# Optimization experiments

Hardware: AMD Instinct MI355X
Metric: run time of the kernel (lower is better)

## Reference

```python
import jax, jax.numpy as jnp
import numpy as np

B, T, D = 4, 4096, 2048
K = 1024
H, KVH, HD = 16, 4, 128
FF = 8192
EPS = 1e-6


def _rmsnorm(x, w):
    v = jnp.mean(x * x, axis=-1, keepdims=True)
    return x * jax.lax.rsqrt(v + EPS) * w


def _rotate_half(x):
    x1, x2 = jnp.split(x, 2, axis=-1)
    return jnp.concatenate([-x2, x1], axis=-1)


def setup_inputs() -> dict:
    key = jax.random.key(0)
    ks = jax.random.split(key, 16)
    hidden_states = jax.random.normal(ks[0], (B, T, D), dtype=jnp.float32)
    # unique sorted indices per sequence (top-k selection without duplicates)
    scores = jax.random.uniform(ks[1], (B, T))
    topk_indices = jnp.sort(jax.lax.top_k(scores, K)[1], axis=-1).astype(jnp.int64)
    gating_scores = jax.random.uniform(ks[2], (B, K), dtype=jnp.float32)
    # rotary embeddings over the full sequence [B, T, HD]
    inv = 1.0 / (10000.0 ** (jnp.arange(0, HD, 2, dtype=jnp.float32) / HD))
    ang = jnp.arange(T, dtype=jnp.float32)[:, None] * inv[None, :]  # [T, HD/2]
    emb = jnp.concatenate([ang, ang], axis=-1)
    cos = jnp.broadcast_to(jnp.cos(emb)[None], (B, T, HD)).astype(jnp.float32)
    sin = jnp.broadcast_to(jnp.sin(emb)[None], (B, T, HD)).astype(jnp.float32)
    s = 0.02
    params = dict(
        Wq=jax.random.normal(ks[3], (D, H * HD)) * s,
        bq=jnp.zeros((H * HD,)),
        Wk=jax.random.normal(ks[4], (D, KVH * HD)) * s,
        bk=jnp.zeros((KVH * HD,)),
        Wv=jax.random.normal(ks[5], (D, KVH * HD)) * s,
        bv=jnp.zeros((KVH * HD,)),
        Wo=jax.random.normal(ks[6], (H * HD, D)) * s,
        w_gate=jax.random.normal(ks[7], (D, FF)) * s,
        w_up=jax.random.normal(ks[8], (D, FF)) * s,
        w_down=jax.random.normal(ks[9], (FF, D)) * s,
        ln1_w=jnp.ones((D,)),
        ln2_w=jnp.ones((D,)),
    )
    return dict(hidden_states=hidden_states, topk_indices=topk_indices,
                gating_scores=gating_scores, cos=cos, sin=sin, **params)


def _decoder_layer(x, cos_s, sin_s, Wq, bq, Wk, bk, Wv, bv, Wo,
                   w_gate, w_up, w_down, ln1_w, ln2_w):
    # x: [B, K, D]; cos_s/sin_s: [B, K, HD]
    res = x
    h = _rmsnorm(x, ln1_w)
    q = (h @ Wq + bq).reshape(B, K, H, HD)
    k = (h @ Wk + bk).reshape(B, K, KVH, HD)
    v = (h @ Wv + bv).reshape(B, K, KVH, HD)
    c = cos_s[:, :, None, :]
    s = sin_s[:, :, None, :]
    q = q * c + _rotate_half(q) * s
    k = k * c + _rotate_half(k) * s
    # GQA: repeat kv heads
    k = jnp.repeat(k, H // KVH, axis=2)
    v = jnp.repeat(v, H // KVH, axis=2)
    scores = jnp.einsum('bqhd,bkhd->bhqk', q, k) / np.sqrt(HD)
    causal = jnp.tril(jnp.ones((K, K), dtype=bool))
    scores = jnp.where(causal[None, None], scores, jnp.finfo(scores.dtype).min)
    attn = jax.nn.softmax(scores, axis=-1)
    out = jnp.einsum('bhqk,bkhd->bqhd', attn, v).reshape(B, K, H * HD)
    x = res + out @ Wo
    # MLP (SwiGLU)
    res = x
    h = _rmsnorm(x, ln2_w)
    x = res + (jax.nn.silu(h @ w_gate) * (h @ w_up)) @ w_down
    return x


def reference(hidden_states, topk_indices, gating_scores, cos, sin,
              Wq, bq, Wk, bk, Wv, bv, Wo, w_gate, w_up, w_down, ln1_w, ln2_w):
    idx = topk_indices[:, :, None]  # [B, K, 1]
    selected = jnp.take_along_axis(hidden_states, idx, axis=1)  # [B, K, D]
    cos_s = jnp.take_along_axis(cos, idx, axis=1)
    sin_s = jnp.take_along_axis(sin, idx, axis=1)
    processed = _decoder_layer(selected, cos_s, sin_s, Wq, bq, Wk, bk, Wv, bv,
                               Wo, w_gate, w_up, w_down, ln1_w, ln2_w)
    # soft gating: selected + gate * (processed - selected)
    updated = selected + (processed - selected) * gating_scores[:, :, None]
    b_idx = jnp.arange(B)[:, None]
    final = hidden_states.at[b_idx, topk_indices].set(updated)
    return final
```

## Files before the change

kernel.cpp:

```cpp
#include <hip/hip_runtime.h>
#include <stdint.h>

typedef __bf16 bf16;
typedef __attribute__((ext_vector_type(8))) __bf16 bf16x8;
typedef __attribute__((ext_vector_type(4))) float f32x4;

namespace {

constexpr int cB = 4, cT = 4096, cD = 2048, cK = 1024, cH = 16, cKVH = 4, cHD = 128, cFF = 8192;
constexpr int cM = cB * cK;
constexpr int QKVW = cH * cHD + 2 * cKVH * cHD;

__device__ __forceinline__ void load_lds16(const void* g, void* l) {
  __builtin_amdgcn_global_load_lds((const __attribute__((address_space(1))) void*)g,
                                   (__attribute__((address_space(3))) void*)l, 16, 0, 0);
}

template <int N>
__device__ __forceinline__ void waitcnt_vm() {
  if constexpr (N == 0) asm volatile("s_waitcnt vmcnt(0)" ::: "memory");
  else if constexpr (N == 3) asm volatile("s_waitcnt vmcnt(3)" ::: "memory");
  else if constexpr (N == 4) asm volatile("s_waitcnt vmcnt(4)" ::: "memory");
  else if constexpr (N == 6) asm volatile("s_waitcnt vmcnt(6)" ::: "memory");
  else if constexpr (N == 8) asm volatile("s_waitcnt vmcnt(8)" ::: "memory");
  else if constexpr (N == 9) asm volatile("s_waitcnt vmcnt(9)" ::: "memory");
  else if constexpr (N == 12) asm volatile("s_waitcnt vmcnt(12)" ::: "memory");
  else static_assert(N == 0, "unsupported vmcnt literal");
}

template <int OP>
__device__ __forceinline__ float blk_reduce(float v) {
  __shared__ float sm[5];
  const int tid = threadIdx.x, lane = tid & 63, wid = tid >> 6;
#pragma unroll
  for (int o = 32; o; o >>= 1) {
    float o2 = __shfl_down(v, o, 64);
    v = OP ? fmaxf(v, o2) : v + o2;
  }
  if (lane == 0) sm[wid] = v;
  __syncthreads();
  if (tid == 0) {
    float r = sm[0];
#pragma unroll
    for (int i = 1; i < 4; ++i) r = OP ? fmaxf(r, sm[i]) : r + sm[i];
    sm[4] = r;
  }
  __syncthreads();
  float r = sm[4];
  __syncthreads();
  return r;
}

template <int BN, int WM, int WN, int RING, int UNROLL, class Epi>
__global__ __launch_bounds__(512, 2)
void gemm256(const bf16* __restrict__ A, int lda,
             const bf16* __restrict__ Bm, int ldb,
             int Kd, int GM, Epi epi) {
  constexpr int BM = 256;
  constexpr int FM = BM / WM / 16;
  constexpr int FN = BN / WN / 16;
  constexpr int ACALLS = 2;
  constexpr int BCALLS = BN / 128;
  constexpr int L = ACALLS + BCALLS;
  constexpr int D = RING - 1;
  constexpr int SLOTA = BM * 64;
  constexpr int SLOTB = BN * 64;
  constexpr int SLOT = SLOTA + SLOTB;
  __shared__ __align__(16) char lds[RING * SLOT];

  const int tid = threadIdx.x;
  const int lane = tid & 63;
  const int wid = tid >> 6;
  const int l15 = lane & 15, lq = lane >> 4;
  const int wr = wid / WN, wc = wid % WN;

  const int nwg = gridDim.x;
  const int xcd = blockIdx.x & 7, loc = blockIdx.x >> 3;
  const int wg = xcd * (nwg >> 3) + loc;
  const int GN = nwg / GM;
  const int per = 8 * GN;
  const int g = wg / per, r = wg % per;
  const int bm = g * 8 + (r & 7);
  const int bn = r >> 3;

  const bf16* Abase = A + (int64_t)bm * BM * lda;
  const bf16* Bbase = Bm + (int64_t)bn * BN * ldb;

  const bf16* srcA[ACALLS];
  int dstA[ACALLS];
#pragma unroll
  for (int c2 = 0; c2 < ACALLS; ++c2) {
    const int chunk = c2 * 512 + tid;
    const int row = chunk >> 2, pc = chunk & 3;
    const int lc = pc ^ ((row >> 1) & 3);
    srcA[c2] = Abase + (int64_t)row * lda + lc * 8;
    dstA[c2] = chunk * 16;
  }
  const bf16* srcB[BCALLS];
  int dstB[BCALLS];
#pragma unroll
  for (int c2 = 0; c2 < BCALLS; ++c2) {
    const int chunk = c2 * 512 + tid;
    const int row = chunk >> 2, pc = chunk & 3;
    const int lc = pc ^ ((row >> 1) & 3);
    srcB[c2] = Bbase + (int64_t)row * ldb + lc * 8;
    dstB[c2] = chunk * 16;
  }

  int offA[FM], offB[FN];
#pragma unroll
  for (int m = 0; m < FM; ++m) {
    const int row = wr * (BM / WM) + m * 16 + l15;
    offA[m] = row * 64 + (lq ^ ((row >> 1) & 3)) * 16;
  }
#pragma unroll
  for (int n = 0; n < FN; ++n) {
    const int row = wc * (BN / WN) + n * 16 + l15;
    offB[n] = SLOTA + row * 64 + (lq ^ ((row >> 1) & 3)) * 16;
  }

  const int KT = Kd >> 5;
  auto stage = [&](int t) {
    char* sb = lds + (size_t)(t % RING) * SLOT;
#pragma unroll
    for (int c2 = 0; c2 < ACALLS; ++c2)
      load_lds16(srcA[c2] + t * 32, sb + dstA[c2]);
#pragma unroll
    for (int c2 = 0; c2 < BCALLS; ++c2)
      load_lds16(srcB[c2] + t * 32, sb + SLOTA + dstB[c2]);
  };
  auto compute = [&](int t, f32x4 (&acc)[FM][FN]) {
    const char* sb = lds + (size_t)(t % RING) * SLOT;
    bf16x8 av[FM], bv[FN];
#pragma unroll
    for (int m = 0; m < FM; ++m) av[m] = *(const bf16x8*)(sb + offA[m]);
#pragma unroll
    for (int n = 0; n < FN; ++n) bv[n] = *(const bf16x8*)(sb + offB[n]);
    __builtin_amdgcn_s_setprio(1);
#pragma unroll
    for (int m = 0; m < FM; ++m)
#pragma unroll
      for (int n = 0; n < FN; ++n)
        acc[m][n] = __builtin_amdgcn_mfma_f32_16x16x32_bf16(av[m], bv[n], acc[m][n], 0, 0, 0);
    __builtin_amdgcn_s_setprio(0);
  };

  f32x4 acc[FM][FN] = {};

  if constexpr (UNROLL == 1) {
#pragma unroll
    for (int i = 0; i < D; ++i) stage(i);
    waitcnt_vm<(D - 1) * L>();
    __builtin_amdgcn_s_barrier();
    __builtin_amdgcn_sched_barrier(0);
    for (int t = 0; t < KT - D; ++t) {
      stage(t + D);
      compute(t, acc);
      waitcnt_vm<(D - 1) * L>();
      __builtin_amdgcn_s_barrier();
      __builtin_amdgcn_sched_barrier(0);
    }
    waitcnt_vm<0>();
    __builtin_amdgcn_s_barrier();
    for (int t = KT - D; t < KT; ++t) compute(t, acc);
  } else {
    static_assert(RING == 5 && UNROLL == 2, "pair mode is RING=5");
#pragma unroll
    for (int i = 0; i < 3; ++i) stage(i);
    waitcnt_vm<L>();
    __builtin_amdgcn_s_barrier();
    __builtin_amdgcn_sched_barrier(0);
    int t = 0;
    for (; t <= KT - 6; t += 2) {
      stage(t + 3);
      stage(t + 4);
      compute(t, acc);
      compute(t + 1, acc);
      waitcnt_vm<L>();
      __builtin_amdgcn_s_barrier();
      __builtin_amdgcn_sched_barrier(0);
    }
    stage(KT - 1);
    waitcnt_vm<0>();
    __builtin_amdgcn_s_barrier();
    compute(KT - 4, acc);
    compute(KT - 3, acc);
    compute(KT - 2, acc);
    compute(KT - 1, acc);
  }

#pragma unroll
  for (int m = 0; m < FM; ++m) {
    const int r0 = bm * BM + wr * (BM / WM) + m * 16 + lq * 4;
#pragma unroll
    for (int n = 0; n < FN; ++n) {
      const int c1 = bn * BN + wc * (BN / WN) + n * 16 + l15;
#pragma unroll
      for (int j = 0; j < 4; ++j) epi(r0 + j, c1, acc[m][n][j]);
    }
  }
}

__global__ __launch_bounds__(512, 2)
void gemm_gateup(const bf16* __restrict__ A, const bf16* __restrict__ Bg,
                 const bf16* __restrict__ Bu, bf16* __restrict__ act) {
  constexpr int BM = 256;
  constexpr int SLOTA = BM * 64;
  __shared__ __align__(16) char lds[4 * SLOTA];

  const int tid = threadIdx.x;
  const int lane = tid & 63;
  const int wid = tid >> 6;
  const int l15 = lane & 15, lq = lane >> 4;
  const int wr = wid >> 2, wc = wid & 3;

  const int nwg = gridDim.x;
  const int xcd = blockIdx.x & 7, loc = blockIdx.x >> 3;
  const int wg = xcd * (nwg >> 3) + loc;
  const int GM = 16, GN = nwg / GM;
  const int per = 8 * GN;
  const int gg = wg / per, r = wg % per;
  const int bm = gg * 8 + (r & 7);
  const int bn = r >> 3;

  const bf16* Abase = A + (int64_t)bm * BM * cD;

  const bf16* srcA[2];
  int dstA[2];
#pragma unroll
  for (int c2 = 0; c2 < 2; ++c2) {
    const int chunk = c2 * 512 + tid;
    const int row = chunk >> 2, pc = chunk & 3;
    const int lc = pc ^ ((row >> 1) & 3);
    srcA[c2] = Abase + (int64_t)row * cD + lc * 8;
    dstA[c2] = chunk * 16;
  }

  const int rk0 = bn * 128 + wc * 32 + l15;
  const bf16* pG = Bg + (int64_t)rk0 * cD + lq * 8;
  const bf16* pU = Bu + (int64_t)rk0 * cD + lq * 8;

  int offA[8];
#pragma unroll
  for (int m = 0; m < 8; ++m) {
    const int row = wr * 128 + m * 16 + l15;
    offA[m] = row * 64 + (lq ^ ((row >> 1) & 3)) * 16;
  }

  const int KT = cD >> 5;
  auto stageA = [&](int t) {
    char* sb = lds + (size_t)(t & 3) * SLOTA;
    load_lds16(srcA[0] + t * 32, sb + dstA[0]);
    load_lds16(srcA[1] + t * 32, sb + dstA[1]);
  };

  f32x4 accg[8][2] = {}, accu[8][2] = {};

  stageA(0);
  stageA(1);
  for (int t = 0; t < KT; ++t) {
    bf16x8 gfr0 = *(const bf16x8*)(pG + t * 32);
    bf16x8 gfr1 = *(const bf16x8*)(pG + t * 32 + 16 * cD);
    bf16x8 ufr0 = *(const bf16x8*)(pU + t * 32);
    bf16x8 ufr1 = *(const bf16x8*)(pU + t * 32 + 16 * cD);
    asm volatile("" ::: "memory");
    if (t + 2 < KT) stageA(t + 2);
    asm volatile("" ::: "memory");
    waitcnt_vm<8>();
    __builtin_amdgcn_s_barrier();
    asm volatile("" ::: "memory");
    const char* sb = lds + (size_t)(t & 3) * SLOTA;
    bf16x8 av[8];
#pragma unroll
    for (int m = 0; m < 8; ++m) av[m] = *(const bf16x8*)(sb + offA[m]);
    __builtin_amdgcn_s_setprio(1);
#pragma unroll
    for (int m = 0; m < 8; ++m) {
      accg[m][0] = __builtin_amdgcn_mfma_f32_16x16x32_bf16(av[m], gfr0, accg[m][0], 0, 0, 0);
      accg[m][1] = __builtin_amdgcn_mfma_f32_16x16x32_bf16(av[m], gfr1, accg[m][1], 0, 0, 0);
      accu[m][0] = __builtin_amdgcn_mfma_f32_16x16x32_bf16(av[m], ufr0, accu[m][0], 0, 0, 0);
      accu[m][1] = __builtin_amdgcn_mfma_f32_16x16x32_bf16(av[m], ufr1, accu[m][1], 0, 0, 0);
    }
    __builtin_amdgcn_s_setprio(0);
  }

#pragma unroll
  for (int m = 0; m < 8; ++m) {
    const int r0 = bm * BM + wr * 128 + m * 16 + lq * 4;
#pragma unroll
    for (int n = 0; n < 2; ++n) {
      const int c1 = bn * 128 + wc * 32 + n * 16 + l15;
#pragma unroll
      for (int j = 0; j < 4; ++j) {
        float gv = accg[m][n][j];
        float s = gv / (1.f + __expf(-gv));
        act[(int64_t)(r0 + j) * cFF + c1] = (bf16)(s * accu[m][n][j]);
      }
    }
  }
}

struct EpiQKV {
  bf16* out; const float* bias;
  __device__ void operator()(int r, int c, float v) const {
    out[(int64_t)r * QKVW + c] = (bf16)(v + bias[c]);
  }
};
struct EpiOProj {
  float* x; const float* hidden; const int* topk;
  __device__ void operator()(int r, int c, float v) const {
    int b = r >> 10;
    int t = topk[r];
    x[(int64_t)r * cD + c] = v + hidden[((int64_t)b * cT + t) * cD + c];
  }
};
struct EpiDown {
  float* out; const float* x; const float* hidden; const int* topk; const float* gating;
  __device__ void operator()(int r, int c, float v) const {
    int b = r >> 10;
    int t = topk[r];
    float x2 = v + x[(int64_t)r * cD + c];
    int64_t ho = ((int64_t)b * cT + t) * cD + c;
    float sel = hidden[ho];
    out[ho] = sel + (x2 - sel) * gating[r];
  }
};

__global__ __launch_bounds__(256, 2) void flash_attn(const bf16* __restrict__ qkv,
                                                     const bf16* __restrict__ vt,
                                                     bf16* __restrict__ outb) {
  constexpr int QB = 64, KVB = 128;
  __shared__ __align__(16) char lds[81920];
  char* sK = lds;
  char* sP = lds + 32768;
  char* sV = lds + 49152;

  const int qt = blockIdx.x, h = blockIdx.y, b = blockIdx.z;
  const int kvh = h >> 2;
  const int qlo = qt * QB;
  const int tid = threadIdx.x, lane = tid & 63, wid = tid >> 6;
  const int l15 = lane & 15, lq = lane >> 4;
  const int wid16 = wid * 16;

  const bf16* qbase = qkv + (int64_t)(b * cK + qlo) * QKVW + h * cHD;
  const bf16* kbase = qkv + (int64_t)(b * cK) * QKVW + cH * cHD + kvh * cHD;
  const bf16* vtbase = vt + (int64_t)(b * cKVH + kvh) * cHD * cK;

#pragma unroll
  for (int c2 = 0; c2 < 4; ++c2) {
    int chunk = c2 * 256 + tid;
    int row = chunk >> 4, c16 = chunk & 15;
    load_lds16(qbase + (int64_t)row * QKVW + (c16 ^ (row & 15)) * 8, sK + chunk * 16);
  }
  __syncthreads();
  bf16x8 qf[4];
  {
    const int row = wid16 + l15;
#pragma unroll
    for (int kt = 0; kt < 4; ++kt)
      qf[kt] = *(const bf16x8*)(sK + row * 256 + (((kt * 4 + lq) ^ (row & 15)) * 16));
  }
  __syncthreads();

  f32x4 oacc[8] = {};
  float m_run[4], l_run[4];
#pragma unroll
  for (int j = 0; j < 4; ++j) { m_run[j] = -3.0e38f; l_run[j] = 0.f; }

  const int jmax = (qlo + QB - 1) >> 7;
  const float sl2e = 0.08838834764831845f * 1.44269504088896f;

  for (int jj = 0; jj <= jmax; ++jj) {
#pragma unroll
    for (int c2 = 0; c2 < 8; ++c2) {
      int chunk = c2 * 256 + tid;
      int row = chunk >> 4, c16 = chunk & 15;
      int cs = (c16 ^ (row & 15)) * 8;
      load_lds16(kbase + (int64_t)(jj * KVB + row) * QKVW + cs, sK + chunk * 16);
      load_lds16(vtbase + (int64_t)row * cK + jj * KVB + cs, sV + chunk * 16);
    }
    __syncthreads();

    f32x4 sacc[8] = {};
#pragma unroll
    for (int kt = 0; kt < 4; ++kt) {
      bf16x8 bv[8];
#pragma unroll
      for (int n = 0; n < 8; ++n) {
        int rk = n * 16 + l15;
        bv[n] = *(const bf16x8*)(sK + rk * 256 + (((kt * 4 + lq) ^ (rk & 15)) * 16));
      }
#pragma unroll
      for (int n = 0; n < 8; ++n)
        sacc[n] = __builtin_amdgcn_mfma_f32_16x16x32_bf16(qf[kt], bv[n], sacc[n], 0, 0, 0);
    }

    if (jj == jmax) {
#pragma unroll
      for (int n = 0; n < 8; ++n)
#pragma unroll
        for (int j = 0; j < 4; ++j) {
          int qrow = qlo + wid16 + lq * 4 + j;
          int kcol = jj * KVB + n * 16 + l15;
          if (kcol > qrow) sacc[n][j] = -3.0e38f;
        }
    }

#pragma unroll
    for (int j = 0; j < 4; ++j) {
      float mx = sacc[0][j];
#pragma unroll
      for (int n = 1; n < 8; ++n) mx = fmaxf(mx, sacc[n][j]);
#pragma unroll
      for (int off = 1; off < 16; off <<= 1) mx = fmaxf(mx, __shfl_xor(mx, off, 64));
      float mnew = fmaxf(m_run[j], mx);
      float corr = exp2f((m_run[j] - mnew) * sl2e);
      m_run[j] = mnew;
      float ps = 0.f;
#pragma unroll
      for (int n = 0; n < 8; ++n) {
        float p = exp2f((sacc[n][j] - mnew) * sl2e);
        sacc[n][j] = p;
        ps += p;
      }
#pragma unroll
      for (int off = 1; off < 16; off <<= 1) ps += __shfl_xor(ps, off, 64);
      l_run[j] = l_run[j] * corr + ps;
#pragma unroll
      for (int n = 0; n < 8; ++n) oacc[n][j] *= corr;
    }

#pragma unroll
    for (int n = 0; n < 8; ++n)
#pragma unroll
      for (int j = 0; j < 4; ++j) {
        int row = wid16 + lq * 4 + j;
        int col = n * 16 + l15;
        int c16 = (col >> 3) ^ (row & 15);
        *(bf16*)(sP + row * 256 + c16 * 16 + (col & 7) * 2) = (bf16)sacc[n][j];
      }
    __syncthreads();

#pragma unroll
    for (int kt = 0; kt < 4; ++kt) {
      const int prow = wid16 + l15;
      bf16x8 av = *(const bf16x8*)(sP + prow * 256 + (((kt * 4 + lq) ^ (prow & 15)) * 16));
      bf16x8 bv[8];
#pragma unroll
      for (int n = 0; n < 8; ++n) {
        int rd = n * 16 + l15;
        bv[n] = *(const bf16x8*)(sV + rd * 256 + (((kt * 4 + lq) ^ (rd & 15)) * 16));
      }
#pragma unroll
      for (int n = 0; n < 8; ++n)
        oacc[n] = __builtin_amdgcn_mfma_f32_16x16x32_bf16(av, bv[n], oacc[n], 0, 0, 0);
    }
    __syncthreads();
  }

#pragma unroll
  for (int j = 0; j < 4; ++j) {
    int row = qlo + wid16 + lq * 4 + j;
    float inv = 1.f / l_run[j];
#pragma unroll
    for (int n = 0; n < 8; ++n) {
      int col = h * cHD + n * 16 + l15;
      outb[((int64_t)b * cK + row) * cD + col] = (bf16)(oacc[n][j] * inv);
    }
  }
}

__global__ void copy_skip(const float4* __restrict__ s, float4* __restrict__ d,
                          const unsigned char* __restrict__ flags, int64_t n) {
  int64_t i = (int64_t)blockIdx.x * blockDim.x + threadIdx.x;
  const int64_t st = (int64_t)gridDim.x * blockDim.x;
  for (; i < n; i += st) {
    int row = (int)(i >> 9);
    if (!flags[row]) d[i] = s[i];
  }
}

__global__ void build_flags(const int* __restrict__ topk, unsigned char* __restrict__ flags) {
  int r = blockIdx.x * 256 + threadIdx.x;
  if (r < cM) flags[(r >> 10) * cT + topk[r]] = 1;
}

__global__ void wconv(const float* __restrict__ src, bf16* __restrict__ dst,
                      int R, int C, int coff, int ldd) {
  __shared__ float t[32][33];
  const int c0 = blockIdx.x * 32, r0 = blockIdx.y * 32;
  for (int rr = threadIdx.y; rr < 32; rr += 8)
    t[rr][threadIdx.x] = src[(int64_t)(r0 + rr) * C + c0 + threadIdx.x];
  __syncthreads();
  for (int rr = threadIdx.y; rr < 32; rr += 8)
    dst[(int64_t)(c0 + rr + coff) * ldd + r0 + threadIdx.x] = (bf16)t[threadIdx.x][rr];
}

__global__ void biascat(const float* __restrict__ bq, const float* __restrict__ bk,
                        const float* __restrict__ bv, float* __restrict__ o) {
  int i = blockIdx.x * 256 + threadIdx.x;
  if (i < QKVW) o[i] = (i < 2048) ? bq[i] : (i < 2560 ? bk[i - 2048] : bv[i - 2560]);
}

__global__ void rmsnorm_rows(const float* __restrict__ base, const int* __restrict__ topk,
                             const float* __restrict__ w, bf16* __restrict__ out) {
  const int r = blockIdx.x;
  const float* src;
  if (topk) {
    int t = topk[r];
    src = base + ((int64_t)(r >> 10) * cT + t) * cD;
  } else {
    src = base + (int64_t)r * cD;
  }
  const int tid = threadIdx.x;
  const float4* s4 = (const float4*)src;
  float4 a = s4[tid * 2], b = s4[tid * 2 + 1];
  float ss = a.x * a.x + a.y * a.y + a.z * a.z + a.w * a.w +
             b.x * b.x + b.y * b.y + b.z * b.z + b.w * b.w;
  float tot = blk_reduce<0>(ss);
  float sc = rsqrtf(tot * (1.f / cD) + 1e-6f);
  bf16* o = out + (int64_t)r * cD;
  const int d0 = tid * 8;
  o[d0 + 0] = (bf16)(a.x * sc * w[d0 + 0]);
  o[d0 + 1] = (bf16)(a.y * sc * w[d0 + 1]);
  o[d0 + 2] = (bf16)(a.z * sc * w[d0 + 2]);
  o[d0 + 3] = (bf16)(a.w * sc * w[d0 + 3]);
  o[d0 + 4] = (bf16)(b.x * sc * w[d0 + 4]);
  o[d0 + 5] = (bf16)(b.y * sc * w[d0 + 5]);
  o[d0 + 6] = (bf16)(b.z * sc * w[d0 + 6]);
  o[d0 + 7] = (bf16)(b.w * sc * w[d0 + 7]);
}

__global__ void rope_kernel(bf16* __restrict__ qkv, const float* __restrict__ cosb,
                            const float* __restrict__ sinb, const int* __restrict__ topk) {
  const int r = blockIdx.x;
  const int b = r >> 10;
  const int t = topk[r];
  const float* cr = cosb + ((int64_t)b * cT + t) * cHD;
  const float* sr = sinb + ((int64_t)b * cT + t) * cHD;
  bf16* rowq = qkv + (int64_t)r * QKVW;
  for (int p = threadIdx.x; p < (cH + cKVH) * 64; p += 256) {
    int hh = p >> 6, d = p & 63;
    bf16* base = (hh < cH) ? (rowq + hh * cHD) : (rowq + cH * cHD + (hh - cH) * cHD);
    float x1 = (float)base[d], x2 = (float)base[d + 64];
    float c1 = cr[d], s1 = sr[d], c2 = cr[d + 64], s2 = sr[d + 64];
    base[d] = (bf16)(x1 * c1 - x2 * s1);
    base[d + 64] = (bf16)(x2 * c2 + x1 * s2);
  }
}

__global__ void vtrans(const bf16* __restrict__ qkv, bf16* __restrict__ Vt) {
  __shared__ bf16 t[32][33];
  const int bz = blockIdx.z, b = bz >> 2, kv = bz & 3;
  const int k0 = blockIdx.x * 32, d0 = blockIdx.y * 32;
  for (int rr = threadIdx.y; rr < 32; rr += 8)
    t[rr][threadIdx.x] =
        qkv[(int64_t)(b * cK + k0 + rr) * QKVW + cH * cHD + cKVH * cHD + kv * cHD + d0 + threadIdx.x];
  __syncthreads();
  for (int rr = threadIdx.y; rr < 32; rr += 8)
    Vt[((int64_t)(b * cKVH + kv) * cHD + d0 + rr) * cK + k0 + threadIdx.x] = t[threadIdx.x][rr];
}

}

extern "C" void kernel_launch(void* const* d_in, const int* in_sizes, int n_in,
                              void* d_out, int out_size, void* d_ws, size_t ws_size,
                              hipStream_t stream) {
  const float* hidden = (const float*)d_in[0];
  const int* topk = (const int*)d_in[1];
  const float* gating = (const float*)d_in[2];
  const float* cosb = (const float*)d_in[3];
  const float* sinb = (const float*)d_in[4];
  const float* Wq = (const float*)d_in[5];
  const float* bq = (const float*)d_in[6];
  const float* Wk = (const float*)d_in[7];
  const float* bk = (const float*)d_in[8];
  const float* Wv = (const float*)d_in[9];
  const float* bv = (const float*)d_in[10];
  const float* Wo = (const float*)d_in[11];
  const float* wg = (const float*)d_in[12];
  const float* wu = (const float*)d_in[13];
  const float* wd = (const float*)d_in[14];
  const float* ln1 = (const float*)d_in[15];
  const float* ln2 = (const float*)d_in[16];
  float* out = (float*)d_out;
  (void)in_sizes; (void)n_in; (void)out_size; (void)ws_size;

  char* ws = (char*)d_ws;
  size_t off = 0;
  auto alloc = [&](size_t bytes) {
    char* p = ws + off;
    off += (bytes + 255) & ~(size_t)255;
    return p;
  };
  bf16* wt_qkv = (bf16*)alloc((size_t)QKVW * cD * 2);
  bf16* wt_o = (bf16*)alloc((size_t)cD * cD * 2);
  bf16* wt_g = (bf16*)alloc((size_t)cFF * cD * 2);
  bf16* wt_u = (bf16*)alloc((size_t)cFF * cD * 2);
  bf16* wt_d = (bf16*)alloc((size_t)cD * cFF * 2);
  float* bias_cat = (float*)alloc((size_t)QKVW * 4);
  bf16* hbuf = (bf16*)alloc((size_t)cM * cD * 2);
  bf16* qkv = (bf16*)alloc((size_t)cM * QKVW * 2);
  bf16* vt = (bf16*)alloc((size_t)cB * cKVH * cHD * cK * 2);
  bf16* attnout = (bf16*)alloc((size_t)cM * cD * 2);
  float* xbuf = (float*)alloc((size_t)cM * cD * 4);
  bf16* actbuf = (bf16*)alloc((size_t)cM * cFF * 2);
  unsigned char* flags = (unsigned char*)alloc((size_t)cB * cT);

  hipMemsetAsync(flags, 0, (size_t)cB * cT, stream);
  build_flags<<<cM / 256, 256, 0, stream>>>(topk, flags);
  copy_skip<<<2048, 256, 0, stream>>>((const float4*)hidden, (float4*)out, flags,
                                      (int64_t)cB * cT * cD / 4);

  const dim3 tb(32, 8);
  wconv<<<dim3(cD / 32, cD / 32), tb, 0, stream>>>(Wq, wt_qkv, cD, cD, 0, cD);
  wconv<<<dim3(512 / 32, cD / 32), tb, 0, stream>>>(Wk, wt_qkv, cD, 512, 2048, cD);
  wconv<<<dim3(512 / 32, cD / 32), tb, 0, stream>>>(Wv, wt_qkv, cD, 512, 2560, cD);
  wconv<<<dim3(cD / 32, cD / 32), tb, 0, stream>>>(Wo, wt_o, cD, cD, 0, cD);
  wconv<<<dim3(cFF / 32, cD / 32), tb, 0, stream>>>(wg, wt_g, cD, cFF, 0, cD);
  wconv<<<dim3(cFF / 32, cD / 32), tb, 0, stream>>>(wu, wt_u, cD, cFF, 0, cD);
  wconv<<<dim3(cD / 32, cFF / 32), tb, 0, stream>>>(wd, wt_d, cFF, cD, 0, cFF);
  biascat<<<(QKVW + 255) / 256, 256, 0, stream>>>(bq, bk, bv, bias_cat);

  rmsnorm_rows<<<cM, 256, 0, stream>>>(hidden, topk, ln1, hbuf);
  gemm256<256, 2, 4, 5, 2, EpiQKV><<<16 * (QKVW / 256), 512, 0, stream>>>(
      hbuf, cD, wt_qkv, cD, cD, 16, EpiQKV{qkv, bias_cat});
  rope_kernel<<<cM, 256, 0, stream>>>(qkv, cosb, sinb, topk);
  vtrans<<<dim3(cK / 32, cHD / 32, cB * cKVH), tb, 0, stream>>>(qkv, vt);

  flash_attn<<<dim3(cK / 64, cH, cB), 256, 0, stream>>>(qkv, vt, attnout);

  gemm256<128, 4, 2, 5, 2, EpiOProj><<<16 * (cD / 128), 512, 0, stream>>>(
      attnout, cD, wt_o, cD, cD, 16, EpiOProj{xbuf, hidden, topk});
  rmsnorm_rows<<<cM, 256, 0, stream>>>(xbuf, nullptr, ln2, hbuf);
  gemm_gateup<<<16 * (cFF / 128), 512, 0, stream>>>(hbuf, wt_g, wt_u, actbuf);
  gemm256<128, 4, 2, 5, 2, EpiDown><<<16 * (cD / 128), 512, 0, stream>>>(
      actbuf, cFF, wt_d, cFF, cFF, 16, EpiDown{out, xbuf, hidden, topk, gating});
}
```

Measured before the change: 922.8 us.

## Pre-swizzle gate/up weights into MFMA fragment layout and double-buffer B loads

The gate/up weights are now converted into a fragment-contiguous bf16 layout, so each lane's 16-byte B fragment for a k-step sits next to its neighbours' and a wavefront reads fully coalesced 1KB blocks. The gate/up GEMM main loop is unrolled by two and uses ping-pong registers, issuing the next k-step's B loads before the current MFMAs run. The aim is to hide global-load latency and cut uncoalesced strided reads. The cost is a new conversion kernel with strided fp32 reads and more vector registers, and the waitcnt bookkeeping has to stay matched to the load counts.

```diff
diff --git a/kernel.cpp b/kernel.cpp
--- a/kernel.cpp
+++ b/kernel.cpp
@@ -236,9 +236,12 @@
     dstA[c2] = chunk * 16;
   }
 
-  const int rk0 = bn * 128 + wc * 32 + l15;
-  const bf16* pG = Bg + (int64_t)rk0 * cD + lq * 8;
-  const bf16* pU = Bu + (int64_t)rk0 * cD + lq * 8;
+  const int KT = cD >> 5;
+  const int nb0 = bn * 8 + wc * 2;
+  const bf16* pG0 = Bg + ((int64_t)nb0 * KT * 64 + lane) * 8;
+  const bf16* pG1 = Bg + ((int64_t)(nb0 + 1) * KT * 64 + lane) * 8;
+  const bf16* pU0 = Bu + ((int64_t)nb0 * KT * 64 + lane) * 8;
+  const bf16* pU1 = Bu + ((int64_t)(nb0 + 1) * KT * 64 + lane) * 8;
 
   int offA[8];
 #pragma unroll
@@ -247,7 +250,6 @@
     offA[m] = row * 64 + (lq ^ ((row >> 1) & 3)) * 16;
   }
 
-  const int KT = cD >> 5;
   auto stageA = [&](int t) {
     char* sb = lds + (size_t)(t & 3) * SLOTA;
     load_lds16(srcA[0] + t * 32, sb + dstA[0]);
@@ -255,33 +257,45 @@
   };
 
   f32x4 accg[8][2] = {}, accu[8][2] = {};
-
+  bf16x8 gA0, gA1, uA0, uA1, gB0, gB1, uB0, uB1;
+
+  auto loadB = [&](int t, bf16x8& g0, bf16x8& g1, bf16x8& u0, bf16x8& u1) {
+    g0 = *(const bf16x8*)(pG0 + (int64_t)t * 512);
+    g1 = *(const bf16x8*)(pG1 + (int64_t)t * 512);
+    u0 = *(const bf16x8*)(pU0 + (int64_t)t * 512);
+    u1 = *(const bf16x8*)(pU1 + (int64_t)t * 512);
+  };
+  auto mfma_step = [&](const char* sb, const bf16x8& g0, const bf16x8& g1,
+                       const bf16x8& u0, const bf16x8& u1) {
+    bf16x8 av[8];
+#pragma unroll
+    for (int m = 0; m < 8; ++m) av[m] = *(const bf16x8*)(sb + offA[m]);
+    __builtin_amdgcn_s_setprio(1);
+#pragma unroll
+    for (int m = 0; m < 8; ++m) {
+      accg[m][0] = __builtin_amdgcn_mfma_f32_16x16x32_bf16(av[m], g0, accg[m][0], 0, 0, 0);
+      accg[m][1] = __builtin_amdgcn_mfma_f32_16x16x32_bf16(av[m], g1, accg[m][1], 0, 0, 0);
+      accu[m][0] = __builtin_amdgcn_mfma_f32_16x16x32_bf16(av[m], u0, accu[m][0], 0, 0, 0);
+      accu[m][1] = __builtin_amdgcn_mfma_f32_16x16x32_bf16(av[m], u1, accu[m][1], 0, 0, 0);
+    }
+    __builtin_amdgcn_s_setprio(0);
+  };
+
+  loadB(0, gA0, gA1, uA0, uA1);
   stageA(0);
   stageA(1);
-  for (int t = 0; t < KT; ++t) {
-    bf16x8 gfr0 = *(const bf16x8*)(pG + t * 32);
-    bf16x8 gfr1 = *(const bf16x8*)(pG + t * 32 + 16 * cD);
-    bf16x8 ufr0 = *(const bf16x8*)(pU + t * 32);
-    bf16x8 ufr1 = *(const bf16x8*)(pU + t * 32 + 16 * cD);
-    asm volatile("" ::: "memory");
+  for (int t = 0; t < KT; t += 2) {
+    loadB(t + 1, gB0, gB1, uB0, uB1);
     if (t + 2 < KT) stageA(t + 2);
-    asm volatile("" ::: "memory");
     waitcnt_vm<8>();
     __builtin_amdgcn_s_barrier();
-    asm volatile("" ::: "memory");
-    const char* sb = lds + (size_t)(t & 3) * SLOTA;
-    bf16x8 av[8];
-#pragma unroll
-    for (int m = 0; m < 8; ++m) av[m] = *(const bf16x8*)(sb + offA[m]);
-    __builtin_amdgcn_s_setprio(1);
-#pragma unroll
-    for (int m = 0; m < 8; ++m) {
-      accg[m][0] = __builtin_amdgcn_mfma_f32_16x16x32_bf16(av[m], gfr0, accg[m][0], 0, 0, 0);
-      accg[m][1] = __builtin_amdgcn_mfma_f32_16x16x32_bf16(av[m], gfr1, accg[m][1], 0, 0, 0);
-      accu[m][0] = __builtin_amdgcn_mfma_f32_16x16x32_bf16(av[m], ufr0, accu[m][0], 0, 0, 0);
-      accu[m][1] = __builtin_amdgcn_mfma_f32_16x16x32_bf16(av[m], ufr1, accu[m][1], 0, 0, 0);
-    }
-    __builtin_amdgcn_s_setprio(0);
+    mfma_step(lds + (size_t)(t & 3) * SLOTA, gA0, gA1, uA0, uA1);
+    if (t + 2 < KT) loadB(t + 2, gA0, gA1, uA0, uA1);
+    if (t + 3 < KT) stageA(t + 3);
+    if (t + 3 < KT) waitcnt_vm<6>();
+    else            waitcnt_vm<4>();
+    __builtin_amdgcn_s_barrier();
+    mfma_step(lds + (size_t)((t + 1) & 3) * SLOTA, gB0, gB1, uB0, uB1);
   }
 
 #pragma unroll
@@ -494,6 +508,20 @@
   __syncthreads();
   for (int rr = threadIdx.y; rr < 32; rr += 8)
     dst[(int64_t)(c0 + rr + coff) * ldd + r0 + threadIdx.x] = (bf16)t[threadIdx.x][rr];
+}
+
+__global__ void wconv_frag(const float* __restrict__ src, bf16* __restrict__ dst,
+                           int N, int KT) {
+  const int id = blockIdx.x * 256 + threadIdx.x;
+  const int lane = id & 63;
+  const int frag = id >> 6;
+  const int kc = frag % KT;
+  const int nb = frag / KT;
+  const int l15 = lane & 15, lq = lane >> 4;
+  const float* s = src + (int64_t)(kc * 32 + lq * 8) * N + nb * 16 + l15;
+  bf16* o = dst + (int64_t)id * 8;
+#pragma unroll
+  for (int j = 0; j < 8; ++j) o[j] = (bf16)s[(int64_t)j * N];
 }
 
 __global__ void biascat(const float* __restrict__ bq, const float* __restrict__ bk,
@@ -617,8 +645,8 @@
   wconv<<<dim3(512 / 32, cD / 32), tb, 0, stream>>>(Wk, wt_qkv, cD, 512, 2048, cD);
   wconv<<<dim3(512 / 32, cD / 32), tb, 0, stream>>>(Wv, wt_qkv, cD, 512, 2560, cD);
   wconv<<<dim3(cD / 32, cD / 32), tb, 0, stream>>>(Wo, wt_o, cD, cD, 0, cD);
-  wconv<<<dim3(cFF / 32, cD / 32), tb, 0, stream>>>(wg, wt_g, cD, cFF, 0, cD);
-  wconv<<<dim3(cFF / 32, cD / 32), tb, 0, stream>>>(wu, wt_u, cD, cFF, 0, cD);
+  wconv_frag<<<(cFF / 16) * (cD / 32) * 64 / 256, 256, 0, stream>>>(wg, wt_g, cFF, cD / 32);
+  wconv_frag<<<(cFF / 16) * (cD / 32) * 64 / 256, 256, 0, stream>>>(wu, wt_u, cFF, cD / 32);
   wconv<<<dim3(cD / 32, cFF / 32), tb, 0, stream>>>(wd, wt_d, cFF, cD, 0, cFF);
   biascat<<<(QKVW + 255) / 256, 256, 0, stream>>>(bq, bk, bv, bias_cat);
 
```

New measurement: 855.9 us. -7.2%, faster.

## Rewrite gate/up GEMM with interleaved weights and LDS-staged 256x256 tiles

Applied to the files above, without the earlier changes.

The gate and up weights are converted into one interleaved bf16 matrix, with 16-row blocks of gate and up alternating. The gate/up GEMM is rewritten to stage both A and B tiles (256x256, K-step 64) into double-buffered swizzled LDS. Loads for the next step are interleaved with four MFMA quadrant phases separated by barriers. This replaces direct global B-fragment loads, improving B reuse across waves and hiding load latency, at the cost of more barriers and LDS use. The flash attention grid is also remapped so that blocks sharing a KV head are grouped per XCD for L2 locality.

```diff
diff --git a/kernel.cpp b/kernel.cpp
--- a/kernel.cpp
+++ b/kernel.cpp
@@ -19,12 +19,11 @@
 template <int N>
 __device__ __forceinline__ void waitcnt_vm() {
   if constexpr (N == 0) asm volatile("s_waitcnt vmcnt(0)" ::: "memory");
+  else if constexpr (N == 2) asm volatile("s_waitcnt vmcnt(2)" ::: "memory");
   else if constexpr (N == 3) asm volatile("s_waitcnt vmcnt(3)" ::: "memory");
   else if constexpr (N == 4) asm volatile("s_waitcnt vmcnt(4)" ::: "memory");
   else if constexpr (N == 6) asm volatile("s_waitcnt vmcnt(6)" ::: "memory");
   else if constexpr (N == 8) asm volatile("s_waitcnt vmcnt(8)" ::: "memory");
-  else if constexpr (N == 9) asm volatile("s_waitcnt vmcnt(9)" ::: "memory");
-  else if constexpr (N == 12) asm volatile("s_waitcnt vmcnt(12)" ::: "memory");
   else static_assert(N == 0, "unsupported vmcnt literal");
 }
 
@@ -202,14 +201,12 @@
 }
 
 __global__ __launch_bounds__(512, 2)
-void gemm_gateup(const bf16* __restrict__ A, const bf16* __restrict__ Bg,
-                 const bf16* __restrict__ Bu, bf16* __restrict__ act) {
-  constexpr int BM = 256;
-  constexpr int SLOTA = BM * 64;
-  __shared__ __align__(16) char lds[4 * SLOTA];
-
-  const int tid = threadIdx.x;
-  const int lane = tid & 63;
+void gemm_gateup8(const bf16* __restrict__ A, const bf16* __restrict__ Bgu,
+                  bf16* __restrict__ act) {
+  constexpr int QSZ = 64 * 128;
+  __shared__ __align__(16) char lds[2 * 8 * QSZ];
+
+  const int tid = threadIdx.x, lane = tid & 63;
   const int wid = tid >> 6;
   const int l15 = lane & 15, lq = lane >> 4;
   const int wr = wid >> 2, wc = wid & 3;
@@ -219,82 +216,111 @@
   const int wg = xcd * (nwg >> 3) + loc;
   const int GM = 16, GN = nwg / GM;
   const int per = 8 * GN;
-  const int gg = wg / per, r = wg % per;
-  const int bm = gg * 8 + (r & 7);
+  const int g = wg / per, r = wg % per;
+  const int bm = g * 8 + (r & 7);
   const int bn = r >> 3;
 
-  const bf16* Abase = A + (int64_t)bm * BM * cD;
-
-  const bf16* srcA[2];
-  int dstA[2];
-#pragma unroll
-  for (int c2 = 0; c2 < 2; ++c2) {
-    const int chunk = c2 * 512 + tid;
-    const int row = chunk >> 2, pc = chunk & 3;
-    const int lc = pc ^ ((row >> 1) & 3);
-    srcA[c2] = Abase + (int64_t)row * cD + lc * 8;
-    dstA[c2] = chunk * 16;
-  }
-
-  const int rk0 = bn * 128 + wc * 32 + l15;
-  const bf16* pG = Bg + (int64_t)rk0 * cD + lq * 8;
-  const bf16* pU = Bu + (int64_t)rk0 * cD + lq * 8;
-
-  int offA[8];
+  const bf16* Abase = A + (int64_t)bm * 256 * cD;
+  const bf16* Bbase = Bgu + (int64_t)bn * 256 * cD;
+
+  const int srow = tid >> 3, spc = tid & 7;
+  const int slc = spc ^ (srow & 7);
+  const int sdst = tid * 16;
+  const bf16* qsrc[8];
+#pragma unroll
+  for (int q = 0; q < 4; ++q) qsrc[q] = Abase + (int64_t)(q * 64 + srow) * cD + slc * 8;
+#pragma unroll
+  for (int q = 0; q < 4; ++q) qsrc[4 + q] = Bbase + (int64_t)(q * 64 + srow) * cD + slc * 8;
+
+  auto stageQ = [&](int buf, int q, int kt) {
+    load_lds16(qsrc[q] + kt * 64, lds + (size_t)(buf * 8 + q) * QSZ + sdst);
+  };
+
+  f32x4 acc[8][4] = {};
+  bf16x8 af[4][2], bfr[2][2];
+
+  auto ldA = [&](int buf, int qr) {
+    const char* qb = lds + (size_t)(buf * 8 + wr * 2 + qr) * QSZ;
+#pragma unroll
+    for (int mq = 0; mq < 4; ++mq) {
+      const int rr = mq * 16 + l15;
+#pragma unroll
+      for (int ks = 0; ks < 2; ++ks)
+        af[mq][ks] = *(const bf16x8*)(qb + rr * 128 + (((ks * 4 + lq) ^ (rr & 7)) * 16));
+    }
+  };
+  auto ldB = [&](int buf, int qc) {
+    const char* qb = lds + (size_t)(buf * 8 + 4 + wc) * QSZ;
+#pragma unroll
+    for (int nq = 0; nq < 2; ++nq) {
+      const int rr = qc * 32 + nq * 16 + l15;
+#pragma unroll
+      for (int ks = 0; ks < 2; ++ks)
+        bfr[nq][ks] = *(const bf16x8*)(qb + rr * 128 + (((ks * 4 + lq) ^ (rr & 7)) * 16));
+    }
+  };
+  auto mfma16 = [&](int qr, int qc) {
+    __builtin_amdgcn_s_setprio(1);
+#pragma unroll
+    for (int ks = 0; ks < 2; ++ks)
+#pragma unroll
+      for (int mq = 0; mq < 4; ++mq)
+#pragma unroll
+        for (int nq = 0; nq < 2; ++nq)
+          acc[qr * 4 + mq][qc * 2 + nq] = __builtin_amdgcn_mfma_f32_16x16x32_bf16(
+              af[mq][ks], bfr[nq][ks], acc[qr * 4 + mq][qc * 2 + nq], 0, 0, 0);
+    __builtin_amdgcn_s_setprio(0);
+  };
+
+  const int KT = cD >> 6;
+
+  stageQ(0, 4, 0); stageQ(0, 5, 0);
+  stageQ(0, 6, 0); stageQ(0, 7, 0);
+  stageQ(0, 0, 0); stageQ(0, 2, 0);
+  stageQ(0, 1, 0); stageQ(0, 3, 0);
+  waitcnt_vm<2>();
+  __builtin_amdgcn_s_barrier();
+
+  for (int t = 0; t < KT; ++t) {
+    const int buf = t & 1, nb = buf ^ 1;
+    const bool more = (t + 1 < KT);
+    ldA(buf, 0);
+    ldB(buf, 0);
+    if (more) { stageQ(nb, 4, t + 1); stageQ(nb, 5, t + 1); }
+    __builtin_amdgcn_s_barrier();
+    mfma16(0, 0);
+    __builtin_amdgcn_s_barrier();
+    ldB(buf, 1);
+    if (more) { stageQ(nb, 6, t + 1); stageQ(nb, 7, t + 1); }
+    __builtin_amdgcn_s_barrier();
+    mfma16(0, 1);
+    if (more) waitcnt_vm<4>();
+    else      waitcnt_vm<0>();
+    __builtin_amdgcn_s_barrier();
+    ldA(buf, 1);
+    if (more) { stageQ(nb, 0, t + 1); stageQ(nb, 2, t + 1); }
+    __builtin_amdgcn_s_barrier();
+    mfma16(1, 1);
+    __builtin_amdgcn_s_barrier();
+    ldB(buf, 0);
+    if (more) { stageQ(nb, 1, t + 1); stageQ(nb, 3, t + 1); }
+    __builtin_amdgcn_s_barrier();
+    mfma16(1, 0);
+    if (more) waitcnt_vm<2>();
+    __builtin_amdgcn_s_barrier();
+  }
+
 #pragma unroll
   for (int m = 0; m < 8; ++m) {
-    const int row = wr * 128 + m * 16 + l15;
-    offA[m] = row * 64 + (lq ^ ((row >> 1) & 3)) * 16;
-  }
-
-  const int KT = cD >> 5;
-  auto stageA = [&](int t) {
-    char* sb = lds + (size_t)(t & 3) * SLOTA;
-    load_lds16(srcA[0] + t * 32, sb + dstA[0]);
-    load_lds16(srcA[1] + t * 32, sb + dstA[1]);
-  };
-
-  f32x4 accg[8][2] = {}, accu[8][2] = {};
-
-  stageA(0);
-  stageA(1);
-  for (int t = 0; t < KT; ++t) {
-    bf16x8 gfr0 = *(const bf16x8*)(pG + t * 32);
-    bf16x8 gfr1 = *(const bf16x8*)(pG + t * 32 + 16 * cD);
-    bf16x8 ufr0 = *(const bf16x8*)(pU + t * 32);
-    bf16x8 ufr1 = *(const bf16x8*)(pU + t * 32 + 16 * cD);
-    asm volatile("" ::: "memory");
-    if (t + 2 < KT) stageA(t + 2);
-    asm volatile("" ::: "memory");
-    waitcnt_vm<8>();
-    __builtin_amdgcn_s_barrier();
-    asm volatile("" ::: "memory");
-    const char* sb = lds + (size_t)(t & 3) * SLOTA;
-    bf16x8 av[8];
-#pragma unroll
-    for (int m = 0; m < 8; ++m) av[m] = *(const bf16x8*)(sb + offA[m]);
-    __builtin_amdgcn_s_setprio(1);
-#pragma unroll
-    for (int m = 0; m < 8; ++m) {
-      accg[m][0] = __builtin_amdgcn_mfma_f32_16x16x32_bf16(av[m], gfr0, accg[m][0], 0, 0, 0);
-      accg[m][1] = __builtin_amdgcn_mfma_f32_16x16x32_bf16(av[m], gfr1, accg[m][1], 0, 0, 0);
-      accu[m][0] = __builtin_amdgcn_mfma_f32_16x16x32_bf16(av[m], ufr0, accu[m][0], 0, 0, 0);
-      accu[m][1] = __builtin_amdgcn_mfma_f32_16x16x32_bf16(av[m], ufr1, accu[m][1], 0, 0, 0);
-    }
-    __builtin_amdgcn_s_setprio(0);
-  }
-
-#pragma unroll
-  for (int m = 0; m < 8; ++m) {
-    const int r0 = bm * BM + wr * 128 + m * 16 + lq * 4;
-#pragma unroll
-    for (int n = 0; n < 2; ++n) {
-      const int c1 = bn * 128 + wc * 32 + n * 16 + l15;
+    const int row = bm * 256 + wr * 128 + (m >> 2) * 64 + (m & 3) * 16 + lq * 4;
+#pragma unroll
+    for (int p = 0; p < 2; ++p) {
+      const int col = bn * 128 + wc * 32 + p * 16 + l15;
 #pragma unroll
       for (int j = 0; j < 4; ++j) {
-        float gv = accg[m][n][j];
+        float gv = acc[m][2 * p][j];
         float s = gv / (1.f + __expf(-gv));
-        act[(int64_t)(r0 + j) * cFF + c1] = (bf16)(s * accu[m][n][j]);
+        act[(int64_t)(row + j) * cFF + col] = (bf16)(s * acc[m][2 * p + 1][j]);
       }
     }
   }
@@ -335,7 +361,9 @@
   char* sP = lds + 32768;
   char* sV = lds + 49152;
 
-  const int qt = blockIdx.x, h = blockIdx.y, b = blockIdx.z;
+  const int xcdid = blockIdx.x & 7, locid = blockIdx.x >> 3;
+  const int wg = xcdid * 128 + locid;
+  const int qt = wg & 15, h = (wg >> 4) & 15, b = wg >> 8;
   const int kvh = h >> 2;
   const int qlo = qt * QB;
   const int tid = threadIdx.x, lane = tid & 63, wid = tid >> 6;
@@ -494,6 +522,21 @@
   __syncthreads();
   for (int rr = threadIdx.y; rr < 32; rr += 8)
     dst[(int64_t)(c0 + rr + coff) * ldd + r0 + threadIdx.x] = (bf16)t[threadIdx.x][rr];
+}
+
+__global__ void wconv_gu(const float* __restrict__ srcG, const float* __restrict__ srcU,
+                         bf16* __restrict__ dst) {
+  __shared__ float t[32][33];
+  const float* src = blockIdx.z ? srcU : srcG;
+  const int c0 = blockIdx.x * 32, r0 = blockIdx.y * 32;
+  for (int rr = threadIdx.y; rr < 32; rr += 8)
+    t[rr][threadIdx.x] = src[(int64_t)(r0 + rr) * cFF + c0 + threadIdx.x];
+  __syncthreads();
+  for (int rr = threadIdx.y; rr < 32; rr += 8) {
+    int c = c0 + rr;
+    int dr = ((c & ~15) << 1) | (blockIdx.z ? 16 : 0) | (c & 15);
+    dst[(int64_t)dr * cD + r0 + threadIdx.x] = (bf16)t[threadIdx.x][rr];
+  }
 }
 
 __global__ void biascat(const float* __restrict__ bq, const float* __restrict__ bk,
@@ -595,8 +638,7 @@
   };
   bf16* wt_qkv = (bf16*)alloc((size_t)QKVW * cD * 2);
   bf16* wt_o = (bf16*)alloc((size_t)cD * cD * 2);
-  bf16* wt_g = (bf16*)alloc((size_t)cFF * cD * 2);
-  bf16* wt_u = (bf16*)alloc((size_t)cFF * cD * 2);
+  bf16* wt_gu = (bf16*)alloc((size_t)2 * cFF * cD * 2);
   bf16* wt_d = (bf16*)alloc((size_t)cD * cFF * 2);
   float* bias_cat = (float*)alloc((size_t)QKVW * 4);
   bf16* hbuf = (bf16*)alloc((size_t)cM * cD * 2);
@@ -607,7 +649,7 @@
   bf16* actbuf = (bf16*)alloc((size_t)cM * cFF * 2);
   unsigned char* flags = (unsigned char*)alloc((size_t)cB * cT);
 
-  hipMemsetAsync(flags, 0, (size_t)cB * cT, stream);
+  (void)hipMemsetAsync(flags, 0, (size_t)cB * cT, stream);
   build_flags<<<cM / 256, 256, 0, stream>>>(topk, flags);
   copy_skip<<<2048, 256, 0, stream>>>((const float4*)hidden, (float4*)out, flags,
                                       (int64_t)cB * cT * cD / 4);
@@ -617,8 +659,7 @@
   wconv<<<dim3(512 / 32, cD / 32), tb, 0, stream>>>(Wk, wt_qkv, cD, 512, 2048, cD);
   wconv<<<dim3(512 / 32, cD / 32), tb, 0, stream>>>(Wv, wt_qkv, cD, 512, 2560, cD);
   wconv<<<dim3(cD / 32, cD / 32), tb, 0, stream>>>(Wo, wt_o, cD, cD, 0, cD);
-  wconv<<<dim3(cFF / 32, cD / 32), tb, 0, stream>>>(wg, wt_g, cD, cFF, 0, cD);
-  wconv<<<dim3(cFF / 32, cD / 32), tb, 0, stream>>>(wu, wt_u, cD, cFF, 0, cD);
+  wconv_gu<<<dim3(cFF / 32, cD / 32, 2), tb, 0, stream>>>(wg, wu, wt_gu);
   wconv<<<dim3(cD / 32, cFF / 32), tb, 0, stream>>>(wd, wt_d, cFF, cD, 0, cFF);
   biascat<<<(QKVW + 255) / 256, 256, 0, stream>>>(bq, bk, bv, bias_cat);
 
@@ -628,12 +669,12 @@
   rope_kernel<<<cM, 256, 0, stream>>>(qkv, cosb, sinb, topk);
   vtrans<<<dim3(cK / 32, cHD / 32, cB * cKVH), tb, 0, stream>>>(qkv, vt);
 
-  flash_attn<<<dim3(cK / 64, cH, cB), 256, 0, stream>>>(qkv, vt, attnout);
+  flash_attn<<<1024, 256, 0, stream>>>(qkv, vt, attnout);
 
   gemm256<128, 4, 2, 5, 2, EpiOProj><<<16 * (cD / 128), 512, 0, stream>>>(
       attnout, cD, wt_o, cD, cD, 16, EpiOProj{xbuf, hidden, topk});
   rmsnorm_rows<<<cM, 256, 0, stream>>>(xbuf, nullptr, ln2, hbuf);
-  gemm_gateup<<<16 * (cFF / 128), 512, 0, stream>>>(hbuf, wt_g, wt_u, actbuf);
+  gemm_gateup8<<<16 * (2 * cFF / 256), 512, 0, stream>>>(hbuf, wt_gu, actbuf);
   gemm256<128, 4, 2, 5, 2, EpiDown><<<16 * (cD / 128), 512, 0, stream>>>(
       actbuf, cFF, wt_d, cFF, cFF, 16, EpiDown{out, xbuf, hidden, topk, gating});
 }
```

After: 835.8 us, median of 2. 9.4% less time.
